# Optimization experiments

Hardware: AMD Instinct MI355X
Metric: run time of the kernel (lower is better)

## Reference

```python
import jax, jax.numpy as jnp
import numpy as np

V, NJ, NCOMP, NBETA = 778, 16, 24, 10
F_CLOSED, N_ANCHOR = 1554, 32
B, NOBJ = 8, 16384
# MANO kinematic tree parents (wrist + 5 fingers x 3 joints)
PARENTS = np.array([-1, 0, 1, 2, 0, 4, 5, 0, 7, 8, 0, 10, 11, 0, 13, 14])


def setup_inputs() -> dict:
    key = jax.random.key(0)
    ks = jax.random.split(key, 12)
    hand_pose = jax.random.normal(ks[0], (B, 3 + 3 + NCOMP), jnp.float32) * 0.1
    obj_points = jax.random.normal(ks[1], (B, NOBJ, 3), jnp.float32) * 0.1
    hand_beta = jax.random.normal(ks[2], (B, NBETA), jnp.float32) * 0.5
    v_template = jax.random.normal(ks[3], (V, 3), jnp.float32) * 0.05
    shapedirs = jax.random.normal(ks[4], (V, 3, NBETA), jnp.float32) * 0.01
    posedirs = jax.random.normal(ks[5], (V, 3, (NJ - 1) * 9), jnp.float32) * 0.01
    J_regressor = jax.nn.softmax(jax.random.normal(ks[6], (NJ, V), jnp.float32), axis=-1)
    lbs_weights = jax.nn.softmax(jax.random.normal(ks[7], (V, NJ), jnp.float32) * 2.0, axis=-1)
    pca_comps = jax.random.normal(ks[8], (NCOMP, (NJ - 1) * 3), jnp.float32) * 0.1
    anchor_weights = jax.nn.softmax(jax.random.normal(ks[9], (N_ANCHOR, 3), jnp.float32), axis=-1)
    closed_faces = jax.random.randint(ks[10], (F_CLOSED, 3), 0, V, jnp.int32)
    anchor_face_idx = jax.random.randint(ks[11], (N_ANCHOR, 3), 0, V, jnp.int32)
    return dict(hand_pose=hand_pose, obj_points=obj_points, hand_beta=hand_beta,
                v_template=v_template, shapedirs=shapedirs, posedirs=posedirs,
                J_regressor=J_regressor, lbs_weights=lbs_weights, pca_comps=pca_comps,
                anchor_weights=anchor_weights, closed_faces=closed_faces,
                anchor_face_idx=anchor_face_idx)


def rodrigues(r):
    # r: [..., 3] axis-angle -> [..., 3, 3] rotation matrix
    theta = jnp.sqrt(jnp.sum(r * r, axis=-1, keepdims=True) + 1e-16)
    k = r / theta
    c = jnp.cos(theta)[..., None]
    s = jnp.sin(theta)[..., None]
    kx, ky, kz = k[..., 0], k[..., 1], k[..., 2]
    zero = jnp.zeros_like(kx)
    K = jnp.stack([zero, -kz, ky, kz, zero, -kx, -ky, kx, zero], axis=-1)
    K = K.reshape(r.shape[:-1] + (3, 3))
    I = jnp.eye(3, dtype=r.dtype)
    return c * I + s * K + (1.0 - c) * k[..., :, None] * k[..., None, :]


def mano_verts(hand_pose, hand_beta, v_template, shapedirs, posedirs,
               J_regressor, lbs_weights, pca_comps):
    b = hand_pose.shape[0]
    trans = hand_pose[:, :3]
    root = hand_pose[:, 3:6]
    hand45 = hand_pose[:, 6:] @ pca_comps  # PCA -> 45-dim pose (flat_hand_mean: no mean add)
    full = jnp.concatenate([root, hand45], axis=-1).reshape(b, NJ, 3)
    R = rodrigues(full)  # [B,16,3,3]
    v_shaped = v_template + jnp.einsum('vdk,bk->bvd', shapedirs, hand_beta)
    J = jnp.einsum('jv,bvd->bjd', J_regressor, v_shaped)  # [B,16,3]
    pose_feat = (R[:, 1:] - jnp.eye(3, dtype=R.dtype)).reshape(b, (NJ - 1) * 9)
    v_posed = v_shaped + jnp.einsum('vdp,bp->bvd', posedirs, pose_feat)

    def make44(Rj, tj):  # [B,3,3],[B,3] -> [B,4,4]
        T = jnp.zeros((b, 4, 4), R.dtype)
        return T.at[:, :3, :3].set(Rj).at[:, :3, 3].set(tj).at[:, 3, 3].set(1.0)

    Ts = [make44(R[:, 0], J[:, 0])]
    for j in range(1, NJ):  # fixed small kinematic chain
        p = int(PARENTS[j])
        Ts.append(jnp.einsum('bmn,bnk->bmk', Ts[p], make44(R[:, j], J[:, j] - J[:, p])))
    T = jnp.stack(Ts, axis=1)  # [B,16,4,4] global joint transforms
    corr = jnp.einsum('bjmn,bjn->bjm', T[..., :3, :3], J)
    A = T.at[..., :3, 3].add(-corr)  # relative-to-rest transforms
    Tw = jnp.einsum('vj,bjmn->bvmn', lbs_weights, A)  # per-vertex skinning transform
    verts = jnp.einsum('bvmn,bvn->bvm', Tw[..., :3, :3], v_posed) + Tw[..., :3, 3]
    return verts + trans[:, None, :]


def vertex_normals(verts, faces):  # verts [B,V,3], faces [F,3]
    def one(v):
        p0, p1, p2 = v[faces[:, 0]], v[faces[:, 1]], v[faces[:, 2]]
        fn = jnp.cross(p1 - p0, p2 - p0)
        vn = (jnp.zeros_like(v).at[faces[:, 0]].add(fn)
              .at[faces[:, 1]].add(fn).at[faces[:, 2]].add(fn))
        return vn / (jnp.linalg.norm(vn, axis=-1, keepdims=True) + 1e-8)
    return jax.vmap(one)(verts)


def reference(hand_pose, obj_points, hand_beta, v_template, shapedirs, posedirs,
              J_regressor, lbs_weights, pca_comps, anchor_weights,
              closed_faces, anchor_face_idx):
    verts = mano_verts(hand_pose, hand_beta, v_template, shapedirs, posedirs,
                       J_regressor, lbs_weights, pca_comps)  # [B,778,3]
    # get_NN: squared cdist obj->hand + argmin (the memory-bound bottleneck)
    d2 = (jnp.sum(obj_points * obj_points, -1, keepdims=True)
          + jnp.sum(verts * verts, -1)[:, None, :]
          - 2.0 * jnp.einsum('bnd,bvd->bnv', obj_points, verts))  # [B,NOBJ,778]
    nn_idx = jnp.argmin(d2, axis=-1)  # [B,NOBJ]
    nn_dist = jnp.take_along_axis(d2, nn_idx[..., None], axis=-1)[..., 0]
    # contact_map_of_m_to_n
    cmap = 1.0 - 2.0 * (jax.nn.sigmoid(100.0 * nn_dist) - 0.5)
    # inter_penetr_loss: interior obj points (behind nearest hand vertex normal)
    normals = vertex_normals(verts, closed_faces)
    nn_vert = jnp.take_along_axis(verts, nn_idx[..., None], axis=1)
    nn_norm = jnp.take_along_axis(normals, nn_idx[..., None], axis=1)
    interior = jnp.sum((nn_vert - obj_points) * nn_norm, axis=-1) > 0.0
    penetration = jnp.sum(jnp.where(interior, nn_dist, 0.0)) / hand_pose.shape[0]
    # AnchorLayer: barycentric anchor points on the hand surface
    contact_candidates = jnp.einsum('ak,bakd->bad', anchor_weights, verts[:, anchor_face_idx])
    return cmap, penetration, verts, contact_candidates
```

## Files before the change

kernel.cpp:

```cpp
#include <hip/hip_runtime.h>
#include <math.h>

#define NV 778
#define NJ 16
#define NCOMP 24
#define NBETA 10
#define FC 1554
#define NA 32
#define NB 8
#define NOBJ 16384
#define VD (NV*3)
#define BCH 584

__global__ __launch_bounds__(64) void k_pose(
    const float* __restrict__ hp, const float* __restrict__ pca,
    float* __restrict__ sRg, float* __restrict__ PFg, float* __restrict__ pen)
{
    int b = blockIdx.x, t = threadIdx.x;
    __shared__ float h45[45];
    __shared__ float sR[NJ*9];
    if (t < 45) {
        float acc = 0.0f;
        for (int k = 0; k < NCOMP; ++k) acc += hp[b*30 + 6 + k] * pca[k*45 + t];
        h45[t] = acc;
    }
    __syncthreads();
    if (t < NJ) {
        float rx, ry, rz;
        if (t == 0) { rx = hp[b*30+3]; ry = hp[b*30+4]; rz = hp[b*30+5]; }
        else        { rx = h45[(t-1)*3]; ry = h45[(t-1)*3+1]; rz = h45[(t-1)*3+2]; }
        float th = sqrtf(rx*rx + ry*ry + rz*rz + 1e-16f);
        float kx = rx/th, ky = ry/th, kz = rz/th;
        float c = cosf(th), s = sinf(th), o = 1.0f - c;
        float R[9];
        R[0] = c + o*kx*kx;      R[1] = -s*kz + o*kx*ky;  R[2] =  s*ky + o*kx*kz;
        R[3] =  s*kz + o*ky*kx;  R[4] = c + o*ky*ky;      R[5] = -s*kx + o*ky*kz;
        R[6] = -s*ky + o*kz*kx;  R[7] =  s*kx + o*kz*ky;  R[8] = c + o*kz*kz;
        #pragma unroll
        for (int i = 0; i < 9; ++i) { sR[t*9+i] = R[i]; sRg[b*(NJ*9) + t*9 + i] = R[i]; }
    }
    __syncthreads();
    for (int e = t; e < 135; e += 64) {
        int mn = e % 9;
        float d = (mn == 0 || mn == 4 || mn == 8) ? 1.0f : 0.0f;
        PFg[b*135 + e] = sR[9 + e] - d;
    }
    if (b == 0 && t == 0) *pen = 0.0f;
}

__global__ __launch_bounds__(256) void k_blend(
    const float* __restrict__ vt, const float* __restrict__ sd,
    const float* __restrict__ pd, const float* __restrict__ beta,
    const float* __restrict__ PFg, float* __restrict__ VS, float* __restrict__ VP)
{
    int b = blockIdx.x / BCH, c = blockIdx.x % BCH;
    int wid = threadIdx.x >> 6, lane = threadIdx.x & 63;
    int r = c*4 + wid;
    if (r >= VD) return;

    const float* p  = pd  + r * 135;
    const float* pf = PFg + b * 135;
    float accP = p[lane] * pf[lane] + p[lane+64] * pf[lane+64];
    accP += (lane < 7) ? p[lane+128] * pf[lane+128] : 0.0f;

    float accS = (lane < NBETA) ? sd[r*NBETA + lane] * beta[b*NBETA + lane] : 0.0f;

    #pragma unroll
    for (int off = 32; off; off >>= 1) {
        accP += __shfl_down(accP, off, 64);
        accS += __shfl_down(accS, off, 64);
    }
    if (lane == 0) {
        float vs = vt[r] + accS;
        VS[b*VD + r] = vs;
        VP[b*VD + r] = vs + accP;
    }
}

__global__ __launch_bounds__(1024) void k_skel(
    const float* __restrict__ hp, const float* __restrict__ sRg,
    const float* __restrict__ Jreg, const float* __restrict__ VS,
    const float* __restrict__ VP, const float* __restrict__ W,
    const int* __restrict__ faces, const float* __restrict__ aw,
    const int* __restrict__ afi,
    float* __restrict__ verts, float4* __restrict__ PK,
    float* __restrict__ NRM, float* __restrict__ contact)
{
    int b = blockIdx.x, t = threadIdx.x;
    int lane = t & 63, wid = t >> 6;
    __shared__ float sR[NJ*9];
    __shared__ float sJ[NJ*3];
    __shared__ float4 sA4[NJ*3];
    __shared__ float sv[VD];
    __shared__ float sn[VD];

    if (t < NJ*9) sR[t] = sRg[b*NJ*9 + t];
    for (int i = t; i < VD; i += 1024) sn[i] = 0.0f;

    {
        float a0 = 0.0f, a1 = 0.0f, a2 = 0.0f;
        for (int v = lane; v < NV; v += 64) {
            const float* p = VS + b*VD + v*3;
            float w = Jreg[wid*NV + v];
            a0 += w*p[0]; a1 += w*p[1]; a2 += w*p[2];
        }
        #pragma unroll
        for (int off = 32; off; off >>= 1) {
            a0 += __shfl_down(a0, off, 64);
            a1 += __shfl_down(a1, off, 64);
            a2 += __shfl_down(a2, off, 64);
        }
        if (lane == 0) {
            sJ[wid*3+0] = a0; sJ[wid*3+1] = a1; sJ[wid*3+2] = a2;
        }
    }
    __syncthreads();

    if (t < 3) {
        const int par[NJ] = {-1,0,1,2,0,4,5,0,7,8,0,10,11,0,13,14};
        int m = t;
        float Tr[NJ][3], Tt[NJ];
        Tr[0][0] = sR[m*3+0]; Tr[0][1] = sR[m*3+1]; Tr[0][2] = sR[m*3+2];
        Tt[0] = sJ[m];
        #pragma unroll
        for (int j = 1; j < NJ; ++j) {
            int p = par[j];
            float t0 = sJ[j*3+0] - sJ[p*3+0];
            float t1 = sJ[j*3+1] - sJ[p*3+1];
            float t2 = sJ[j*3+2] - sJ[p*3+2];
            float a0 = Tr[p][0], a1 = Tr[p][1], a2 = Tr[p][2];
            #pragma unroll
            for (int n = 0; n < 3; ++n)
                Tr[j][n] = a0*sR[j*9+n] + a1*sR[j*9+3+n] + a2*sR[j*9+6+n];
            Tt[j] = a0*t0 + a1*t1 + a2*t2 + Tt[p];
        }
        #pragma unroll
        for (int j = 0; j < NJ; ++j) {
            float corr = Tr[j][0]*sJ[j*3] + Tr[j][1]*sJ[j*3+1] + Tr[j][2]*sJ[j*3+2];
            sA4[j*3 + m] = make_float4(Tr[j][0], Tr[j][1], Tr[j][2], Tt[j] - corr);
        }
    }
    __syncthreads();

    float tx = hp[b*30+0], ty = hp[b*30+1], tz = hp[b*30+2];
    for (int v = t; v < NV; v += 1024) {
        float4 r0 = make_float4(0,0,0,0), r1 = make_float4(0,0,0,0), r2 = make_float4(0,0,0,0);
        const float* w = W + v * NJ;
        for (int j = 0; j < NJ; ++j) {
            float wj = w[j];
            float4 A0 = sA4[j*3+0], A1 = sA4[j*3+1], A2 = sA4[j*3+2];
            r0.x += wj*A0.x; r0.y += wj*A0.y; r0.z += wj*A0.z; r0.w += wj*A0.w;
            r1.x += wj*A1.x; r1.y += wj*A1.y; r1.z += wj*A1.z; r1.w += wj*A1.w;
            r2.x += wj*A2.x; r2.y += wj*A2.y; r2.z += wj*A2.z; r2.w += wj*A2.w;
        }
        int i = b*NV + v;
        float px = VP[b*VD + v*3], py = VP[b*VD + v*3+1], pz = VP[b*VD + v*3+2];
        float x = r0.x*px + r0.y*py + r0.z*pz + r0.w + tx;
        float y = r1.x*px + r1.y*py + r1.z*pz + r1.w + ty;
        float z = r2.x*px + r2.y*py + r2.z*pz + r2.w + tz;
        sv[v*3] = x; sv[v*3+1] = y; sv[v*3+2] = z;
        verts[i*3] = x; verts[i*3+1] = y; verts[i*3+2] = z;
        PK[i] = make_float4(x, y, z, 0.5f*(x*x + y*y + z*z));
    }
    __syncthreads();

    for (int f = t; f < FC; f += 1024) {
        int i0 = faces[f*3], i1 = faces[f*3+1], i2 = faces[f*3+2];
        float ax = sv[i1*3+0]-sv[i0*3+0], ay = sv[i1*3+1]-sv[i0*3+1], az = sv[i1*3+2]-sv[i0*3+2];
        float bx = sv[i2*3+0]-sv[i0*3+0], by = sv[i2*3+1]-sv[i0*3+1], bz = sv[i2*3+2]-sv[i0*3+2];
        float cx = ay*bz - az*by, cy = az*bx - ax*bz, cz = ax*by - ay*bx;
        atomicAdd(&sn[i0*3+0], cx); atomicAdd(&sn[i0*3+1], cy); atomicAdd(&sn[i0*3+2], cz);
        atomicAdd(&sn[i1*3+0], cx); atomicAdd(&sn[i1*3+1], cy); atomicAdd(&sn[i1*3+2], cz);
        atomicAdd(&sn[i2*3+0], cx); atomicAdd(&sn[i2*3+1], cy); atomicAdd(&sn[i2*3+2], cz);
    }
    __syncthreads();

    for (int i = t; i < VD; i += 1024) NRM[b*VD + i] = sn[i];
    if (t < NA*3) {
        int a = t / 3, d = t % 3;
        float acc = 0.0f;
        #pragma unroll
        for (int k = 0; k < 3; ++k)
            acc += aw[a*3 + k] * sv[afi[a*3 + k]*3 + d];
        contact[b*NA*3 + t] = acc;
    }
}

__global__ __launch_bounds__(256) void k_nn(const float* __restrict__ obj,
                                            const float4* __restrict__ PK,
                                            const float* __restrict__ NRM,
                                            float* __restrict__ cmap,
                                            float* __restrict__ pen)
{
    int b = blockIdx.x >> 6;
    int n = (blockIdx.x & 63) * 256 + threadIdx.x;
    int t = threadIdx.x, lane = t & 63;
    int base = b * NV;

    __shared__ float4 sPK[NV];
    for (int i = t; i < NV; i += 256) sPK[i] = PK[base + i];
    __syncthreads();

    const float* o = obj + (b*NOBJ + n)*3;
    float ox = o[0], oy = o[1], oz = o[2];

    float sb = 1e30f;
    int jb = 0;
    #pragma unroll 4
    for (int j = 0; j < NV; ++j) {
        float4 v = sPK[j];
        float s = fmaf(-ox, v.x, v.w);
        s = fmaf(-oy, v.y, s);
        s = fmaf(-oz, v.z, s);
        if (s < sb) { sb = s; jb = j; }
    }

    float osq = ox*ox + oy*oy + oz*oz;
    float d2 = 2.0f * sb + osq;
    cmap[b*NOBJ + n] = 2.0f / (1.0f + expf(100.0f * d2));

    float4 qq = sPK[jb];
    float nx = NRM[(base + jb)*3 + 0];
    float ny = NRM[(base + jb)*3 + 1];
    float nz = NRM[(base + jb)*3 + 2];
    float dotp = (qq.x - ox)*nx + (qq.y - oy)*ny + (qq.z - oz)*nz;
    float p = (dotp > 0.0f) ? d2 : 0.0f;
    for (int off = 32; off; off >>= 1) p += __shfl_down(p, off, 64);
    __shared__ float wsum[4];
    if (lane == 0) wsum[t >> 6] = p;
    __syncthreads();
    if (t == 0) atomicAdd(pen, (wsum[0] + wsum[1] + wsum[2] + wsum[3]) * (1.0f / NB));
}

extern "C" void kernel_launch(void* const* d_in, const int* in_sizes, int n_in,
                              void* d_out, int out_size, void* d_ws, size_t ws_size,
                              hipStream_t stream)
{
    const float* hp    = (const float*)d_in[0];
    const float* obj   = (const float*)d_in[1];
    const float* beta  = (const float*)d_in[2];
    const float* vt    = (const float*)d_in[3];
    const float* sd    = (const float*)d_in[4];
    const float* pd    = (const float*)d_in[5];
    const float* Jreg  = (const float*)d_in[6];
    const float* W     = (const float*)d_in[7];
    const float* pca   = (const float*)d_in[8];
    const float* aw    = (const float*)d_in[9];
    const int*   faces = (const int*)d_in[10];
    const int*   afi   = (const int*)d_in[11];

    float* out     = (float*)d_out;
    float* cmap    = out;
    float* pen     = out + NB*NOBJ;
    float* verts   = out + NB*NOBJ + 1;
    float* contact = out + NB*NOBJ + 1 + NB*NV*3;

    float* ws   = (float*)d_ws;
    float4* PK  = (float4*)ws;
    float* NRM  = ws + NB*NV*4;
    float* VS   = NRM + NB*VD;
    float* VP   = VS + NB*VD;
    float* sRg  = VP + NB*VD;
    float* PFg  = sRg + NB*NJ*9;

    k_pose <<<NB, 64, 0, stream>>>(hp, pca, sRg, PFg, pen);
    k_blend<<<NB*BCH, 256, 0, stream>>>(vt, sd, pd, beta, PFg, VS, VP);
    k_skel <<<NB, 1024, 0, stream>>>(hp, sRg, Jreg, VS, VP, W, faces, aw, afi,
                                     verts, PK, NRM, contact);
    k_nn   <<<NB*64, 256, 0, stream>>>(obj, PK, NRM, cmap, pen);
}
```

Measured before the change: 149.1 us.

## Fuse pose computation into blend kernel and split NN argmin into four chains

Removes the separate pose kernel by having every blend block recompute the PCA pose and rotation matrices into shared memory, eliminating one launch and a global round-trip for the pose features. The nearest-neighbour search now runs four independent min/argmin chains over padded shared vertices to increase instruction-level parallelism, merged with first-index tie-breaking. It also switches to fast exp for the contact map. The cost is redundant pose work in every blend block and extra registers in the NN loop.

```diff
diff --git a/kernel.cpp b/kernel.cpp
--- a/kernel.cpp
+++ b/kernel.cpp
@@ -12,15 +12,23 @@
 #define VD (NV*3)
 #define BCH 584
 
-__global__ __launch_bounds__(64) void k_pose(
+__global__ __launch_bounds__(256) void k_blend(
     const float* __restrict__ hp, const float* __restrict__ pca,
-    float* __restrict__ sRg, float* __restrict__ PFg, float* __restrict__ pen)
-{
-    int b = blockIdx.x, t = threadIdx.x;
+    const float* __restrict__ vt, const float* __restrict__ sd,
+    const float* __restrict__ pd, const float* __restrict__ beta,
+    float* __restrict__ VS, float* __restrict__ VP,
+    float* __restrict__ sRg, float* __restrict__ pen)
+{
+    int b = blockIdx.x / BCH, c = blockIdx.x % BCH;
+    int t = threadIdx.x;
+    int wid = t >> 6, lane = t & 63;
     __shared__ float h45[45];
     __shared__ float sR[NJ*9];
+    __shared__ float spf[135];
+
     if (t < 45) {
         float acc = 0.0f;
+        #pragma unroll
         for (int k = 0; k < NCOMP; ++k) acc += hp[b*30 + 6 + k] * pca[k*45 + t];
         h45[t] = acc;
     }
@@ -31,49 +39,45 @@
         else        { rx = h45[(t-1)*3]; ry = h45[(t-1)*3+1]; rz = h45[(t-1)*3+2]; }
         float th = sqrtf(rx*rx + ry*ry + rz*rz + 1e-16f);
         float kx = rx/th, ky = ry/th, kz = rz/th;
-        float c = cosf(th), s = sinf(th), o = 1.0f - c;
+        float cc = cosf(th), s = sinf(th), o = 1.0f - cc;
         float R[9];
-        R[0] = c + o*kx*kx;      R[1] = -s*kz + o*kx*ky;  R[2] =  s*ky + o*kx*kz;
-        R[3] =  s*kz + o*ky*kx;  R[4] = c + o*ky*ky;      R[5] = -s*kx + o*ky*kz;
-        R[6] = -s*ky + o*kz*kx;  R[7] =  s*kx + o*kz*ky;  R[8] = c + o*kz*kz;
-        #pragma unroll
-        for (int i = 0; i < 9; ++i) { sR[t*9+i] = R[i]; sRg[b*(NJ*9) + t*9 + i] = R[i]; }
-    }
-    __syncthreads();
-    for (int e = t; e < 135; e += 64) {
-        int mn = e % 9;
+        R[0] = cc + o*kx*kx;     R[1] = -s*kz + o*kx*ky;  R[2] =  s*ky + o*kx*kz;
+        R[3] =  s*kz + o*ky*kx;  R[4] = cc + o*ky*ky;     R[5] = -s*kx + o*ky*kz;
+        R[6] = -s*ky + o*kz*kx;  R[7] =  s*kx + o*kz*ky;  R[8] = cc + o*kz*kz;
+        #pragma unroll
+        for (int i = 0; i < 9; ++i) sR[t*9+i] = R[i];
+        if (c == 0) {
+            #pragma unroll
+            for (int i = 0; i < 9; ++i) sRg[b*(NJ*9) + t*9 + i] = R[i];
+        }
+    }
+    __syncthreads();
+    if (t < 135) {
+        int mn = t % 9;
         float d = (mn == 0 || mn == 4 || mn == 8) ? 1.0f : 0.0f;
-        PFg[b*135 + e] = sR[9 + e] - d;
-    }
-    if (b == 0 && t == 0) *pen = 0.0f;
-}
-
-__global__ __launch_bounds__(256) void k_blend(
-    const float* __restrict__ vt, const float* __restrict__ sd,
-    const float* __restrict__ pd, const float* __restrict__ beta,
-    const float* __restrict__ PFg, float* __restrict__ VS, float* __restrict__ VP)
-{
-    int b = blockIdx.x / BCH, c = blockIdx.x % BCH;
-    int wid = threadIdx.x >> 6, lane = threadIdx.x & 63;
+        spf[t] = sR[9 + t] - d;
+    }
+    if (b == 0 && c == 0 && t == 0) *pen = 0.0f;
+    __syncthreads();
+
     int r = c*4 + wid;
-    if (r >= VD) return;
-
-    const float* p  = pd  + r * 135;
-    const float* pf = PFg + b * 135;
-    float accP = p[lane] * pf[lane] + p[lane+64] * pf[lane+64];
-    accP += (lane < 7) ? p[lane+128] * pf[lane+128] : 0.0f;
-
-    float accS = (lane < NBETA) ? sd[r*NBETA + lane] * beta[b*NBETA + lane] : 0.0f;
-
-    #pragma unroll
-    for (int off = 32; off; off >>= 1) {
-        accP += __shfl_down(accP, off, 64);
-        accS += __shfl_down(accS, off, 64);
-    }
-    if (lane == 0) {
-        float vs = vt[r] + accS;
-        VS[b*VD + r] = vs;
-        VP[b*VD + r] = vs + accP;
+    if (r < VD) {
+        const float* p  = pd + r * 135;
+        float accP = p[lane] * spf[lane] + p[lane+64] * spf[lane+64];
+        accP += (lane < 7) ? p[lane+128] * spf[lane+128] : 0.0f;
+
+        float accS = (lane < NBETA) ? sd[r*NBETA + lane] * beta[b*NBETA + lane] : 0.0f;
+
+        #pragma unroll
+        for (int off = 32; off; off >>= 1) {
+            accP += __shfl_down(accP, off, 64);
+            accS += __shfl_down(accS, off, 64);
+        }
+        if (lane == 0) {
+            float vs = vt[r] + accS;
+            VS[b*VD + r] = vs;
+            VP[b*VD + r] = vs + accP;
+        }
     }
 }
 
@@ -197,32 +201,51 @@
     int t = threadIdx.x, lane = t & 63;
     int base = b * NV;
 
-    __shared__ float4 sPK[NV];
-    for (int i = t; i < NV; i += 256) sPK[i] = PK[base + i];
+    __shared__ float4 sPK[780];
+    for (int i = t; i < 780; i += 256)
+        sPK[i] = (i < NV) ? PK[base + i] : make_float4(0.f, 0.f, 0.f, 1e30f);
     __syncthreads();
 
     const float* o = obj + (b*NOBJ + n)*3;
     float ox = o[0], oy = o[1], oz = o[2];
 
-    float sb = 1e30f;
-    int jb = 0;
-    #pragma unroll 4
-    for (int j = 0; j < NV; ++j) {
-        float4 v = sPK[j];
-        float s = fmaf(-ox, v.x, v.w);
-        s = fmaf(-oy, v.y, s);
-        s = fmaf(-oz, v.z, s);
-        if (s < sb) { sb = s; jb = j; }
-    }
+    float s0 = 1e30f, s1 = 1e30f, s2 = 1e30f, s3 = 1e30f;
+    int j0 = 0, j1 = 195, j2 = 390, j3 = 585;
+    #pragma unroll 2
+    for (int j = 0; j < 195; ++j) {
+        {
+            float4 v = sPK[j];
+            float s = fmaf(-ox, v.x, v.w); s = fmaf(-oy, v.y, s); s = fmaf(-oz, v.z, s);
+            if (s < s0) { s0 = s; j0 = j; }
+        }
+        {
+            float4 v = sPK[j + 195];
+            float s = fmaf(-ox, v.x, v.w); s = fmaf(-oy, v.y, s); s = fmaf(-oz, v.z, s);
+            if (s < s1) { s1 = s; j1 = j + 195; }
+        }
+        {
+            float4 v = sPK[j + 390];
+            float s = fmaf(-ox, v.x, v.w); s = fmaf(-oy, v.y, s); s = fmaf(-oz, v.z, s);
+            if (s < s2) { s2 = s; j2 = j + 390; }
+        }
+        {
+            float4 v = sPK[j + 585];
+            float s = fmaf(-ox, v.x, v.w); s = fmaf(-oy, v.y, s); s = fmaf(-oz, v.z, s);
+            if (s < s3) { s3 = s; j3 = j + 585; }
+        }
+    }
+    if (s1 < s0) { s0 = s1; j0 = j1; }
+    if (s2 < s0) { s0 = s2; j0 = j2; }
+    if (s3 < s0) { s0 = s3; j0 = j3; }
 
     float osq = ox*ox + oy*oy + oz*oz;
-    float d2 = 2.0f * sb + osq;
-    cmap[b*NOBJ + n] = 2.0f / (1.0f + expf(100.0f * d2));
-
-    float4 qq = sPK[jb];
-    float nx = NRM[(base + jb)*3 + 0];
-    float ny = NRM[(base + jb)*3 + 1];
-    float nz = NRM[(base + jb)*3 + 2];
+    float d2 = 2.0f * s0 + osq;
+    cmap[b*NOBJ + n] = 2.0f / (1.0f + __expf(100.0f * d2));
+
+    float4 qq = sPK[j0];
+    float nx = NRM[(base + j0)*3 + 0];
+    float ny = NRM[(base + j0)*3 + 1];
+    float nz = NRM[(base + j0)*3 + 2];
     float dotp = (qq.x - ox)*nx + (qq.y - oy)*ny + (qq.z - oz)*nz;
     float p = (dotp > 0.0f) ? d2 : 0.0f;
     for (int off = 32; off; off >>= 1) p += __shfl_down(p, off, 64);
@@ -261,10 +284,8 @@
     float* VS   = NRM + NB*VD;
     float* VP   = VS + NB*VD;
     float* sRg  = VP + NB*VD;
-    float* PFg  = sRg + NB*NJ*9;
-
-    k_pose <<<NB, 64, 0, stream>>>(hp, pca, sRg, PFg, pen);
-    k_blend<<<NB*BCH, 256, 0, stream>>>(vt, sd, pd, beta, PFg, VS, VP);
+
+    k_blend<<<NB*BCH, 256, 0, stream>>>(hp, pca, vt, sd, pd, beta, VS, VP, sRg, pen);
     k_skel <<<NB, 1024, 0, stream>>>(hp, sRg, Jreg, VS, VP, W, faces, aw, afi,
                                      verts, PK, NRM, contact);
     k_nn   <<<NB*64, 256, 0, stream>>>(obj, PK, NRM, cmap, pen);
```

Result: no change. 149.2 us (+0.0%).
